# Performance work log

Measured on AMD Instinct MI355X. Metric: run time of the kernel, lower is better.

## Reference

```python
import jax, jax.numpy as jnp
import numpy as np

N_NODES = 50000
N_EDGES = 800000
F_IN = 128
HID = 128
N_CLASSES = 16
SELF_LOOP_W = 2.0  # improved=True -> self-loop fill value 2.0


def _glorot(key, fan_in, fan_out):
    scale = jnp.sqrt(6.0 / (fan_in + fan_out))
    return jax.random.uniform(key, (fan_in, fan_out), jnp.float32, -scale, scale)


def gcn_conv(x, W, b, src, dst, n):
    # PyG GCNConv (improved): out = D^{-1/2} (A + 2I) D^{-1/2} (x W) + b
    h = x @ W                                   # [N, F_out] dense transform
    deg = jnp.zeros((n,), x.dtype).at[dst].add(1.0) + SELF_LOOP_W  # in-degree + 2
    dinv = jax.lax.rsqrt(deg)                   # deg^{-1/2}
    norm = dinv[src] * dinv[dst]                # per-edge coefficient [E]
    msg = h[src] * norm[:, None]                # gather + scale [E, F_out]
    agg = jax.ops.segment_sum(msg, dst, num_segments=n)
    agg = agg + (SELF_LOOP_W * dinv * dinv)[:, None] * h  # self-loop term
    return agg + b


def setup_inputs() -> dict:
    key = jax.random.key(0)
    ks = jax.random.split(key, 10)
    x = jax.random.normal(ks[0], (N_NODES, F_IN), jnp.float32)
    edge_index = jax.random.randint(ks[1], (2, N_EDGES), 0, N_NODES, jnp.int64)
    return {
        "x": x,
        "edge_index": edge_index,
        "W0": _glorot(ks[2], F_IN, HID), "b0": jnp.zeros((HID,), jnp.float32),
        "W1": _glorot(ks[3], HID, HID),  "b1": jnp.zeros((HID,), jnp.float32),
        "W2": _glorot(ks[4], HID, HID),  "b2": jnp.zeros((HID,), jnp.float32),
        "W3": _glorot(ks[5], HID, N_CLASSES), "b3": jnp.zeros((N_CLASSES,), jnp.float32),
    }


def reference(x, edge_index, W0, b0, W1, b1, W2, b2, W3, b3):
    src, dst = edge_index[0], edge_index[1]
    # dropout is identity in eval mode
    h = jax.nn.relu(gcn_conv(x, W0, b0, src, dst, N_NODES))
    h = jax.nn.relu(gcn_conv(h, W1, b1, src, dst, N_NODES))
    h = jax.nn.relu(gcn_conv(h, W2, b2, src, dst, N_NODES))
    return jnp.tanh(gcn_conv(h, W3, b3, src, dst, N_NODES))
```

## Files before the change

### kernel.cpp

```cpp
#include <hip/hip_runtime.h>
#include <hip/hip_fp16.h>
#include <math.h>

#define N_NODES 50000
#define N_EDGES 800000
#define NB 782
#define CH 4096
#define CAP 2048
#define BUCKET_BLOCKS 196
#define CAST_BLOCKS 6250
#define PREPW_BLOCKS 192
#define FILL_GRID (NB + CAST_BLOCKS + PREPW_BLOCKS)
#define FB 1563

typedef _Float16 half8 __attribute__((ext_vector_type(8)));
typedef float floatx4 __attribute__((ext_vector_type(4)));
typedef unsigned uintx4 __attribute__((ext_vector_type(4)));

__global__ __launch_bounds__(256) void k_bucket(const int* __restrict__ src,
                                                const int* __restrict__ dst,
                                                int* __restrict__ gcur,
                                                unsigned* __restrict__ arena) {
    __shared__ int cntA[NB];
    __shared__ int lofs[NB];
    __shared__ int gbase[NB];
    __shared__ int part[256];
    __shared__ unsigned buf[CH];
    const int t = threadIdx.x;
    const int ebase = blockIdx.x * CH;
    const int chunkN = min(CH, N_EDGES - ebase);

    for (int i = t; i < NB; i += 256) cntA[i] = 0;
    __syncthreads();
    for (int i = t; i < chunkN; i += 256)
        atomicAdd(&cntA[dst[ebase + i] >> 6], 1);
    __syncthreads();
    int c[4];
    int s = 0;
#pragma unroll
    for (int q = 0; q < 4; ++q) {
        int idx = t * 4 + q;
        c[q] = (idx < NB) ? cntA[idx] : 0;
        s += c[q];
    }
    part[t] = s;
    __syncthreads();
    for (int d = 1; d < 256; d <<= 1) {
        int u = (t >= d) ? part[t - d] : 0;
        __syncthreads();
        part[t] += u;
        __syncthreads();
    }
    int run = (t > 0) ? part[t - 1] : 0;
#pragma unroll
    for (int q = 0; q < 4; ++q) {
        int idx = t * 4 + q;
        if (idx < NB) {
            lofs[idx] = run;
            run += c[q];
            gbase[idx] = (c[q] > 0) ? atomicAdd(&gcur[idx], c[q]) : 0;
            cntA[idx] = 0;
        }
    }
    __syncthreads();
    for (int i = t; i < chunkN; i += 256) {
        int d = dst[ebase + i];
        int sv = src[ebase + i];
        int b = d >> 6;
        int pos = atomicAdd(&cntA[b], 1);
        buf[lofs[b] + pos] = ((unsigned)d << 16) | (unsigned)sv;
    }
    __syncthreads();
    for (int i = t; i < chunkN; i += 256) {
        unsigned v = buf[i];
        int b = (int)(v >> 16) >> 6;
        int q = i - lofs[b];
        int p = gbase[b] + q;
        if (p < CAP) arena[((size_t)b << 11) + p] = v;
    }
}

__global__ __launch_bounds__(256) void k_fill3prep(
    const unsigned* __restrict__ arena, const int* __restrict__ gcur,
    unsigned* __restrict__ packed, float* __restrict__ dinv,
    unsigned short* __restrict__ eidx, const float* __restrict__ x,
    __half* __restrict__ xh, const float* __restrict__ W0,
    const float* __restrict__ W1, const float* __restrict__ W2,
    __half* __restrict__ WT) {
    const int t = threadIdx.x;
    if (blockIdx.x < NB) {
        const int b = blockIdx.x;
        __shared__ int cnt64[64];
        __shared__ int cur64[64];
        if (t < 64) cnt64[t] = 0;
        __syncthreads();
        const int seglen = min(gcur[b], CAP);
        const unsigned* seg = arena + ((size_t)b << 11);
        for (int i = t; i < seglen; i += 256)
            atomicAdd(&cnt64[(seg[i] >> 16) & 63], 1);
        __syncthreads();
        if (t < 64) {
            int v = cnt64[t];
            int p = v;
#pragma unroll
            for (int d = 1; d < 64; d <<= 1) {
                int u = __shfl_up(p, d, 64);
                if (t >= d) p += u;
            }
            int excl = p - v;
            int node = b * 64 + t;
            if (node < N_NODES) {
                packed[node] =
                    ((unsigned)((b << 11) + excl) << 11) | (unsigned)v;
                dinv[node] = rsqrtf((float)v + 2.0f);
            }
            cur64[t] = excl;
        }
        __syncthreads();
        const int base = b << 11;
        for (int i = t; i < seglen; i += 256) {
            unsigned v = seg[i];
            int d = (int)(v >> 16) & 63;
            int pos = atomicAdd(&cur64[d], 1);
            eidx[base + pos] = (unsigned short)(v & 0xFFFFu);
        }
    } else if (blockIdx.x < NB + CAST_BLOCKS) {
        int i = (blockIdx.x - NB) * 256 + t;
        float4 v = *(const float4*)&x[(size_t)i * 4];
        union { ushort4 u; __half h[4]; } p;
        p.h[0] = __float2half(v.x); p.h[1] = __float2half(v.y);
        p.h[2] = __float2half(v.z); p.h[3] = __float2half(v.w);
        *(ushort4*)&xh[(size_t)i * 4] = p.u;
    } else {
        int idx = blockIdx.x - NB - CAST_BLOCKS;
        int which = idx >> 6;
        const float* W = (which == 0) ? W0 : (which == 1) ? W1 : W2;
        int i = (idx & 63) * 256 + t;
        int k = i >> 7, n = i & 127;
        int np = ((n & 7) << 4) + (n >> 3);
        WT[which * 128 * 128 + np * 128 + k] = __float2half(W[i]);
    }
}

__device__ __forceinline__ void accs(uint4 ua, uint4 ub, float s, float* acc) {
    union { uint4 u; __half2 h2[4]; } va, vb;
    va.u = ua; vb.u = ub;
#pragma unroll
    for (int q = 0; q < 4; ++q) {
        float2 wa = __half22float2(va.h2[q]);
        float2 wb = __half22float2(vb.h2[q]);
        acc[2 * q]     += s * wa.x;
        acc[2 * q + 1] += s * wa.y;
        acc[8 + 2 * q]     += s * wb.x;
        acc[8 + 2 * q + 1] += s * wb.y;
    }
}

template <bool SC>
__global__ __launch_bounds__(256, 2) void k_fused(
    const __half* __restrict__ pin, const __half* __restrict__ WTl,
    const float* __restrict__ dinv, const unsigned* __restrict__ packed,
    const unsigned short* __restrict__ eidx, const float* __restrict__ bias,
    __half* __restrict__ pout) {
    __shared__ __half tl[32 * 136];
    const int t = threadIdx.x;
    const int node8 = t >> 3;
    const int l8 = t & 7;
    const int r = blockIdx.x * 32 + node8;
    const bool valid = r < N_NODES;

    float acc[16];
#pragma unroll
    for (int j = 0; j < 16; ++j) acc[j] = 0.f;
    int i = 0, end = 0;
    if (valid) {
        const uint4* rp = (const uint4*)&pin[(size_t)r * 128];
        uint4 sa = rp[l8], sb = rp[8 + l8];
        float s2 = SC ? 2.f * dinv[r] : 2.f;
        accs(sa, sb, s2, acc);
        unsigned pk = packed[r];
        i = (int)(pk >> 11);
        end = i + (int)(pk & 2047u);
    }
    for (; i + 8 <= end; i += 8) {
        int my = (int)__builtin_nontemporal_load(&eidx[i + l8]);
        uint4 va[8], vb[8];
        float ds8[8];
#pragma unroll
        for (int j = 0; j < 8; ++j) {
            int s0 = __shfl(my, j, 8);
            const uint4* q = (const uint4*)&pin[(size_t)s0 * 128];
            va[j] = q[l8];
            vb[j] = q[8 + l8];
            if (SC) ds8[j] = dinv[s0];
        }
#pragma unroll
        for (int j = 0; j < 8; ++j)
            accs(va[j], vb[j], SC ? ds8[j] : 1.f, acc);
    }
    if (i < end) {
        int n = end - i;
        int my = (l8 < n) ? (int)eidx[i + l8] : 0;
        for (int j = 0; j < n; ++j) {
            int s0 = __shfl(my, j, 8);
            const uint4* q = (const uint4*)&pin[(size_t)s0 * 128];
            accs(q[l8], q[8 + l8], SC ? dinv[s0] : 1.f, acc);
        }
    }
    {
        union { uintx4 u; __half h[8]; } pa, pb;
#pragma unroll
        for (int j = 0; j < 8; ++j) {
            pa.h[j] = __float2half(acc[j]);
            pb.h[j] = __float2half(acc[8 + j]);
        }
        *(uintx4*)&tl[node8 * 136 + 8 * l8] = pa.u;
        *(uintx4*)&tl[node8 * 136 + 64 + 8 * l8] = pb.u;
    }
    __syncthreads();

    const int wave = t >> 6;
    const int lane = t & 63;
    const int m = lane & 15;
    const int quad = lane >> 4;
    const int rtile = wave >> 1;
    const int ctile = wave & 1;
    floatx4 a4[4] = {};
#pragma unroll
    for (int kb = 0; kb < 4; ++kb) {
        half8 af = *(const half8*)&tl[(rtile * 16 + m) * 136 + quad * 8 + kb * 32];
#pragma unroll
        for (int j = 0; j < 4; ++j) {
            half8 bf = *(const half8*)&WTl[(size_t)(((ctile * 4 + j) * 16 + m)) * 128 +
                                           kb * 32 + quad * 8];
            a4[j] = __builtin_amdgcn_mfma_f32_16x16x32_f16(af, bf, a4[j], 0, 0, 0);
        }
    }
    const int f0 = 8 * m + ctile * 4;
    const float4 bi = *(const float4*)&bias[f0];
    const int nb0 = blockIdx.x * 32 + rtile * 16 + quad * 4;
#pragma unroll
    for (int rr = 0; rr < 4; ++rr) {
        int node = nb0 + rr;
        if (node < N_NODES) {
            float dv = dinv[node];
            union { ushort4 u; __half h[4]; } pk4;
            pk4.h[0] = __float2half(fmaxf(dv * (dv * a4[0][rr] + bi.x), 0.f));
            pk4.h[1] = __float2half(fmaxf(dv * (dv * a4[1][rr] + bi.y), 0.f));
            pk4.h[2] = __float2half(fmaxf(dv * (dv * a4[2][rr] + bi.z), 0.f));
            pk4.h[3] = __float2half(fmaxf(dv * (dv * a4[3][rr] + bi.w), 0.f));
            *(ushort4*)&pout[(size_t)node * 128 + f0] = pk4.u;
        }
    }
}

__global__ __launch_bounds__(256) void k_gemm16(const __half* __restrict__ in,
                                                const float* __restrict__ W,
                                                float* __restrict__ hs) {
    __shared__ float Wt[16 * 132];
    const int tid = threadIdx.x;
    for (int i = tid; i < 128 * 16; i += 256) {
        int k = i >> 4, c = i & 15;
        Wt[c * 132 + k] = W[i];
    }
    __syncthreads();
    int gid = blockIdx.x * 256 + tid;
    int r = gid >> 4, c = gid & 15;
    const __half* arow = &in[(size_t)r * 128];
    const float* wrow = &Wt[c * 132];
    float acc = 0.f;
#pragma unroll
    for (int k0 = 0; k0 < 128; k0 += 8) {
        union { uint4 u; __half2 h2[4]; } p;
        p.u = *(const uint4*)&arow[k0];
#pragma unroll
        for (int q = 0; q < 4; ++q) {
            float2 a = __half22float2(p.h2[q]);
            acc += a.x * wrow[k0 + 2 * q] + a.y * wrow[k0 + 2 * q + 1];
        }
    }
    hs[gid] = acc;
}

__global__ __launch_bounds__(256) void k_gather4(const unsigned* __restrict__ packed,
                                                 const unsigned short* __restrict__ eidx,
                                                 const float* __restrict__ hs,
                                                 const float* __restrict__ dinv,
                                                 const float* __restrict__ bias,
                                                 float* __restrict__ out) {
    int tid = blockIdx.x * 256 + threadIdx.x;
    int r = tid >> 2;
    if (r >= N_NODES) return;
    int l = tid & 3;
    int f = l * 4;
    const float dv = dinv[r];
    const float4 bi = *(const float4*)&bias[f];
    float4 h = *(const float4*)&hs[(size_t)r * 16 + f];
    float ax = 2.f * h.x, ay = 2.f * h.y, az = 2.f * h.z, aw = 2.f * h.w;
    unsigned pk = packed[r];
    int i = (int)(pk >> 11);
    int end = i + (int)(pk & 2047u);
    for (; i + 4 <= end; i += 4) {
        int my = (int)eidx[i + l];
#pragma unroll
        for (int j = 0; j < 4; ++j) {
            int s = __shfl(my, j, 4);
            float4 v = *(const float4*)&hs[(size_t)s * 16 + f];
            ax += v.x; ay += v.y; az += v.z; aw += v.w;
        }
    }
    if (i < end) {
        int n = end - i;
        int my = (l < n) ? (int)eidx[i + l] : 0;
        for (int j = 0; j < n; ++j) {
            int s = __shfl(my, j, 4);
            float4 v = *(const float4*)&hs[(size_t)s * 16 + f];
            ax += v.x; ay += v.y; az += v.z; aw += v.w;
        }
    }
    float v0 = tanhf(dv * ax + bi.x);
    float v1 = tanhf(dv * ay + bi.y);
    float v2 = tanhf(dv * az + bi.z);
    float v3 = tanhf(dv * aw + bi.w);
    floatx4 o = {v0, v1, v2, v3};
    __builtin_nontemporal_store(o, (floatx4*)&out[(size_t)r * 16 + f]);
}

extern "C" void kernel_launch(void* const* d_in, const int* in_sizes, int n_in,
                              void* d_out, int out_size, void* d_ws, size_t ws_size,
                              hipStream_t stream) {
    const float* x  = (const float*)d_in[0];
    const int* ei   = (const int*)d_in[1];
    const float* W0 = (const float*)d_in[2];
    const float* b0 = (const float*)d_in[3];
    const float* W1 = (const float*)d_in[4];
    const float* b1 = (const float*)d_in[5];
    const float* W2 = (const float*)d_in[6];
    const float* b2 = (const float*)d_in[7];
    const float* W3 = (const float*)d_in[8];
    const float* b3 = (const float*)d_in[9];
    const int* src = ei;
    const int* dst = ei + N_EDGES;

    __half* A      = (__half*)d_ws;
    __half* P      = A + (size_t)N_NODES * 128;
    __half* WT     = P + (size_t)N_NODES * 128;
    float*  H16    = (float*)(WT + 3 * 128 * 128);
    float*  dinv   = H16 + (size_t)N_NODES * 16;
    unsigned* packed = (unsigned*)(dinv + N_NODES);
    int*    gcur   = (int*)(packed + N_NODES);
    unsigned short* eidx = (unsigned short*)(gcur + 1024);
    unsigned* arena = (unsigned*)(eidx + NB * CAP);

    (void)hipMemsetAsync(gcur, 0, 1024 * sizeof(int), stream);
    k_bucket<<<BUCKET_BLOCKS, 256, 0, stream>>>(src, dst, gcur, arena);
    k_fill3prep<<<FILL_GRID, 256, 0, stream>>>(arena, gcur, packed, dinv,
                                               eidx, x, A, W0, W1, W2, WT);

    k_fused<true><<<FB, 256, 0, stream>>>(A, WT, dinv, packed, eidx, b0, P);
    k_fused<false><<<FB, 256, 0, stream>>>(P, WT + 128 * 128, dinv, packed,
                                           eidx, b1, A);
    k_fused<false><<<FB, 256, 0, stream>>>(A, WT + 2 * 128 * 128, dinv, packed,
                                           eidx, b2, P);
    k_gemm16<<<N_NODES * 16 / 256, 256, 0, stream>>>(P, W3, H16);
    k_gather4<<<(N_NODES * 4 + 255) / 256, 256, 0, stream>>>(
        packed, eidx, H16, dinv, b3, (float*)d_out);
}
```

Measured before the change: 287.8 us.

## Shrink fused aggregation blocks to 16 nodes with 16 lanes per node

The fused gather+GEMM kernel now handles 16 nodes per block instead of 32, giving each node 16 lanes that each load one 16-byte chunk. This halves the accumulator registers, and the launch-bounds occupancy hint rises from 2 to 8 blocks per SM, so more gather loads can be in flight at once. The MFMA stage is re-tiled so each wave computes two 16-column tiles. The grid doubles to 3125 blocks, which exactly covers 50000 nodes, so the bounds checks are removed. In exchange, each warp-wide gather touches fewer distinct rows, and per-block overhead (W loads, syncs) is amortized over fewer nodes.

```diff
diff --git a/kernel.cpp b/kernel.cpp
--- a/kernel.cpp
+++ b/kernel.cpp
@@ -11,7 +11,7 @@
 #define CAST_BLOCKS 6250
 #define PREPW_BLOCKS 192
 #define FILL_GRID (NB + CAST_BLOCKS + PREPW_BLOCKS)
-#define FB 1563
+#define FB 3125
 
 typedef _Float16 half8 __attribute__((ext_vector_type(8)));
 typedef float floatx4 __attribute__((ext_vector_type(4)));
@@ -142,80 +142,80 @@
     }
 }
 
-__device__ __forceinline__ void accs(uint4 ua, uint4 ub, float s, float* acc) {
-    union { uint4 u; __half2 h2[4]; } va, vb;
-    va.u = ua; vb.u = ub;
-#pragma unroll
-    for (int q = 0; q < 4; ++q) {
-        float2 wa = __half22float2(va.h2[q]);
-        float2 wb = __half22float2(vb.h2[q]);
-        acc[2 * q]     += s * wa.x;
-        acc[2 * q + 1] += s * wa.y;
-        acc[8 + 2 * q]     += s * wb.x;
-        acc[8 + 2 * q + 1] += s * wb.y;
-    }
-}
-
 template <bool SC>
-__global__ __launch_bounds__(256, 2) void k_fused(
+__global__ __launch_bounds__(256, 8) void k_fused(
     const __half* __restrict__ pin, const __half* __restrict__ WTl,
     const float* __restrict__ dinv, const unsigned* __restrict__ packed,
     const unsigned short* __restrict__ eidx, const float* __restrict__ bias,
     __half* __restrict__ pout) {
-    __shared__ __half tl[32 * 136];
+    __shared__ __half tl[16 * 136];
     const int t = threadIdx.x;
-    const int node8 = t >> 3;
-    const int l8 = t & 7;
-    const int r = blockIdx.x * 32 + node8;
-    const bool valid = r < N_NODES;
-
-    float acc[16];
-#pragma unroll
-    for (int j = 0; j < 16; ++j) acc[j] = 0.f;
-    int i = 0, end = 0;
-    if (valid) {
-        const uint4* rp = (const uint4*)&pin[(size_t)r * 128];
-        uint4 sa = rp[l8], sb = rp[8 + l8];
+    const int g = t >> 4;
+    const int l = t & 15;
+    const int r = blockIdx.x * 16 + g;
+    const int e8 = l & 7;
+
+    float acc[8];
+    {
+        uint4 sv = *(const uint4*)&pin[(size_t)r * 128 + l * 8];
         float s2 = SC ? 2.f * dinv[r] : 2.f;
-        accs(sa, sb, s2, acc);
-        unsigned pk = packed[r];
-        i = (int)(pk >> 11);
-        end = i + (int)(pk & 2047u);
-    }
+        union { uint4 u; __half2 h2[4]; } v;
+        v.u = sv;
+#pragma unroll
+        for (int q = 0; q < 4; ++q) {
+            float2 w = __half22float2(v.h2[q]);
+            acc[2 * q] = s2 * w.x;
+            acc[2 * q + 1] = s2 * w.y;
+        }
+    }
+    unsigned pk = packed[r];
+    int i = (int)(pk >> 11);
+    int end = i + (int)(pk & 2047u);
     for (; i + 8 <= end; i += 8) {
-        int my = (int)__builtin_nontemporal_load(&eidx[i + l8]);
-        uint4 va[8], vb[8];
+        int my = (int)__builtin_nontemporal_load(&eidx[i + e8]);
+        uint4 va[8];
         float ds8[8];
 #pragma unroll
         for (int j = 0; j < 8; ++j) {
-            int s0 = __shfl(my, j, 8);
-            const uint4* q = (const uint4*)&pin[(size_t)s0 * 128];
-            va[j] = q[l8];
-            vb[j] = q[8 + l8];
+            int s0 = __shfl(my, j, 16);
+            va[j] = *(const uint4*)&pin[(size_t)s0 * 128 + l * 8];
             if (SC) ds8[j] = dinv[s0];
         }
 #pragma unroll
-        for (int j = 0; j < 8; ++j)
-            accs(va[j], vb[j], SC ? ds8[j] : 1.f, acc);
+        for (int j = 0; j < 8; ++j) {
+            union { uint4 u; __half2 h2[4]; } v;
+            v.u = va[j];
+            float s = SC ? ds8[j] : 1.f;
+#pragma unroll
+            for (int q = 0; q < 4; ++q) {
+                float2 w = __half22float2(v.h2[q]);
+                acc[2 * q] += s * w.x;
+                acc[2 * q + 1] += s * w.y;
+            }
+        }
     }
     if (i < end) {
         int n = end - i;
-        int my = (l8 < n) ? (int)eidx[i + l8] : 0;
+        int my = (e8 < n) ? (int)eidx[i + e8] : 0;
         for (int j = 0; j < n; ++j) {
-            int s0 = __shfl(my, j, 8);
-            const uint4* q = (const uint4*)&pin[(size_t)s0 * 128];
-            accs(q[l8], q[8 + l8], SC ? dinv[s0] : 1.f, acc);
+            int s0 = __shfl(my, j, 16);
+            uint4 u = *(const uint4*)&pin[(size_t)s0 * 128 + l * 8];
+            float s = SC ? dinv[s0] : 1.f;
+            union { uint4 uu; __half2 h2[4]; } v;
+            v.uu = u;
+#pragma unroll
+            for (int q = 0; q < 4; ++q) {
+                float2 w = __half22float2(v.h2[q]);
+                acc[2 * q] += s * w.x;
+                acc[2 * q + 1] += s * w.y;
+            }
         }
     }
     {
-        union { uintx4 u; __half h[8]; } pa, pb;
-#pragma unroll
-        for (int j = 0; j < 8; ++j) {
-            pa.h[j] = __float2half(acc[j]);
-            pb.h[j] = __float2half(acc[8 + j]);
-        }
-        *(uintx4*)&tl[node8 * 136 + 8 * l8] = pa.u;
-        *(uintx4*)&tl[node8 * 136 + 64 + 8 * l8] = pb.u;
+        union { uintx4 u; __half h[8]; } p;
+#pragma unroll
+        for (int j = 0; j < 8; ++j) p.h[j] = __float2half(acc[j]);
+        *(uintx4*)&tl[g * 136 + l * 8] = p.u;
     }
     __syncthreads();
 
@@ -223,34 +223,28 @@
     const int lane = t & 63;
     const int m = lane & 15;
     const int quad = lane >> 4;
-    const int rtile = wave >> 1;
-    const int ctile = wave & 1;
-    floatx4 a4[4] = {};
+    floatx4 a4[2] = {};
 #pragma unroll
     for (int kb = 0; kb < 4; ++kb) {
-        half8 af = *(const half8*)&tl[(rtile * 16 + m) * 136 + quad * 8 + kb * 32];
-#pragma unroll
-        for (int j = 0; j < 4; ++j) {
-            half8 bf = *(const half8*)&WTl[(size_t)(((ctile * 4 + j) * 16 + m)) * 128 +
+        half8 af = *(const half8*)&tl[m * 136 + quad * 8 + kb * 32];
+#pragma unroll
+        for (int j = 0; j < 2; ++j) {
+            half8 bf = *(const half8*)&WTl[(size_t)((2 * wave + j) * 16 + m) * 128 +
                                            kb * 32 + quad * 8];
             a4[j] = __builtin_amdgcn_mfma_f32_16x16x32_f16(af, bf, a4[j], 0, 0, 0);
         }
     }
-    const int f0 = 8 * m + ctile * 4;
-    const float4 bi = *(const float4*)&bias[f0];
-    const int nb0 = blockIdx.x * 32 + rtile * 16 + quad * 4;
+    const int f0 = 8 * m + 2 * wave;
+    const float2 bi = *(const float2*)&bias[f0];
+    const int nb0 = blockIdx.x * 16 + quad * 4;
 #pragma unroll
     for (int rr = 0; rr < 4; ++rr) {
         int node = nb0 + rr;
-        if (node < N_NODES) {
-            float dv = dinv[node];
-            union { ushort4 u; __half h[4]; } pk4;
-            pk4.h[0] = __float2half(fmaxf(dv * (dv * a4[0][rr] + bi.x), 0.f));
-            pk4.h[1] = __float2half(fmaxf(dv * (dv * a4[1][rr] + bi.y), 0.f));
-            pk4.h[2] = __float2half(fmaxf(dv * (dv * a4[2][rr] + bi.z), 0.f));
-            pk4.h[3] = __float2half(fmaxf(dv * (dv * a4[3][rr] + bi.w), 0.f));
-            *(ushort4*)&pout[(size_t)node * 128 + f0] = pk4.u;
-        }
+        float dv = dinv[node];
+        union { unsigned u; __half h[2]; } o;
+        o.h[0] = __float2half(fmaxf(dv * (dv * a4[0][rr] + bi.x), 0.f));
+        o.h[1] = __float2half(fmaxf(dv * (dv * a4[1][rr] + bi.y), 0.f));
+        *(unsigned*)&pout[(size_t)node * 128 + f0] = o.u;
     }
 }
 
```

After: 335.9 us. 1.17x slower.

## Fuse final 128x16 GEMM into layer-3 kernel and move casts into bucket kernel

Applied to the files above, without the earlier changes.

The third GCN layer kernel now also runs the last 128->16 projection with MFMA on its activated tile held in shared memory. It writes H16 directly, so the layer-3 fp16 output no longer makes a global round trip and the separate k_gemm16 launch is gone. The x cast and weight transposes (now including an fp16 transposed W3) move from the fill kernel into the bucket kernel's grid, so they run alongside bucketing. The shared gather loop also drops the nontemporal load hint on edge indices, and the last-layer projection now uses fp16 inputs instead of fp32 weights.

```diff
diff --git a/kernel.cpp b/kernel.cpp
--- a/kernel.cpp
+++ b/kernel.cpp
@@ -10,23 +10,53 @@
 #define BUCKET_BLOCKS 196
 #define CAST_BLOCKS 6250
 #define PREPW_BLOCKS 192
-#define FILL_GRID (NB + CAST_BLOCKS + PREPW_BLOCKS)
+#define W3_BLOCKS 8
+#define BPREP_GRID (BUCKET_BLOCKS + CAST_BLOCKS + PREPW_BLOCKS + W3_BLOCKS)
 #define FB 1563
 
 typedef _Float16 half8 __attribute__((ext_vector_type(8)));
 typedef float floatx4 __attribute__((ext_vector_type(4)));
 typedef unsigned uintx4 __attribute__((ext_vector_type(4)));
 
-__global__ __launch_bounds__(256) void k_bucket(const int* __restrict__ src,
-                                                const int* __restrict__ dst,
-                                                int* __restrict__ gcur,
-                                                unsigned* __restrict__ arena) {
+__global__ __launch_bounds__(256) void k_bucket_prep(
+    const int* __restrict__ src, const int* __restrict__ dst,
+    int* __restrict__ gcur, unsigned* __restrict__ arena,
+    const float* __restrict__ x, __half* __restrict__ xh,
+    const float* __restrict__ W0, const float* __restrict__ W1,
+    const float* __restrict__ W2, const float* __restrict__ W3,
+    __half* __restrict__ WT, __half* __restrict__ WT3) {
+    const int t = threadIdx.x;
+    if (blockIdx.x >= BUCKET_BLOCKS) {
+        int xb = blockIdx.x - BUCKET_BLOCKS;
+        if (xb < CAST_BLOCKS) {
+            int i = xb * 256 + t;
+            float4 v = *(const float4*)&x[(size_t)i * 4];
+            union { ushort4 u; __half h[4]; } p;
+            p.h[0] = __float2half(v.x); p.h[1] = __float2half(v.y);
+            p.h[2] = __float2half(v.z); p.h[3] = __float2half(v.w);
+            *(ushort4*)&xh[(size_t)i * 4] = p.u;
+        } else {
+            int idx = xb - CAST_BLOCKS;
+            if (idx < PREPW_BLOCKS) {
+                int which = idx >> 6;
+                const float* W = (which == 0) ? W0 : (which == 1) ? W1 : W2;
+                int i = (idx & 63) * 256 + t;
+                int k = i >> 7, n = i & 127;
+                int np = ((n & 7) << 4) + (n >> 3);
+                WT[which * 128 * 128 + np * 128 + k] = __float2half(W[i]);
+            } else {
+                int i = (idx - PREPW_BLOCKS) * 256 + t;
+                int n = i >> 7, k = i & 127;
+                WT3[n * 128 + k] = __float2half(W3[k * 16 + n]);
+            }
+        }
+        return;
+    }
     __shared__ int cntA[NB];
     __shared__ int lofs[NB];
     __shared__ int gbase[NB];
     __shared__ int part[256];
     __shared__ unsigned buf[CH];
-    const int t = threadIdx.x;
     const int ebase = blockIdx.x * CH;
     const int chunkN = min(CH, N_EDGES - ebase);
 
@@ -80,65 +110,44 @@
     }
 }
 
-__global__ __launch_bounds__(256) void k_fill3prep(
+__global__ __launch_bounds__(256) void k_fill(
     const unsigned* __restrict__ arena, const int* __restrict__ gcur,
     unsigned* __restrict__ packed, float* __restrict__ dinv,
-    unsigned short* __restrict__ eidx, const float* __restrict__ x,
-    __half* __restrict__ xh, const float* __restrict__ W0,
-    const float* __restrict__ W1, const float* __restrict__ W2,
-    __half* __restrict__ WT) {
+    unsigned short* __restrict__ eidx) {
     const int t = threadIdx.x;
-    if (blockIdx.x < NB) {
-        const int b = blockIdx.x;
-        __shared__ int cnt64[64];
-        __shared__ int cur64[64];
-        if (t < 64) cnt64[t] = 0;
-        __syncthreads();
-        const int seglen = min(gcur[b], CAP);
-        const unsigned* seg = arena + ((size_t)b << 11);
-        for (int i = t; i < seglen; i += 256)
-            atomicAdd(&cnt64[(seg[i] >> 16) & 63], 1);
-        __syncthreads();
-        if (t < 64) {
-            int v = cnt64[t];
-            int p = v;
-#pragma unroll
-            for (int d = 1; d < 64; d <<= 1) {
-                int u = __shfl_up(p, d, 64);
-                if (t >= d) p += u;
-            }
-            int excl = p - v;
-            int node = b * 64 + t;
-            if (node < N_NODES) {
-                packed[node] =
-                    ((unsigned)((b << 11) + excl) << 11) | (unsigned)v;
-                dinv[node] = rsqrtf((float)v + 2.0f);
-            }
-            cur64[t] = excl;
-        }
-        __syncthreads();
-        const int base = b << 11;
-        for (int i = t; i < seglen; i += 256) {
-            unsigned v = seg[i];
-            int d = (int)(v >> 16) & 63;
-            int pos = atomicAdd(&cur64[d], 1);
-            eidx[base + pos] = (unsigned short)(v & 0xFFFFu);
-        }
-    } else if (blockIdx.x < NB + CAST_BLOCKS) {
-        int i = (blockIdx.x - NB) * 256 + t;
-        float4 v = *(const float4*)&x[(size_t)i * 4];
-        union { ushort4 u; __half h[4]; } p;
-        p.h[0] = __float2half(v.x); p.h[1] = __float2half(v.y);
-        p.h[2] = __float2half(v.z); p.h[3] = __float2half(v.w);
-        *(ushort4*)&xh[(size_t)i * 4] = p.u;
-    } else {
-        int idx = blockIdx.x - NB - CAST_BLOCKS;
-        int which = idx >> 6;
-        const float* W = (which == 0) ? W0 : (which == 1) ? W1 : W2;
-        int i = (idx & 63) * 256 + t;
-        int k = i >> 7, n = i & 127;
-        int np = ((n & 7) << 4) + (n >> 3);
-        WT[which * 128 * 128 + np * 128 + k] = __float2half(W[i]);
+    const int b = blockIdx.x;
+    __shared__ int cnt64[64];
+    __shared__ int cur64[64];
+    if (t < 64) cnt64[t] = 0;
+    __syncthreads();
+    const int seglen = min(gcur[b], CAP);
+    const unsigned* seg = arena + ((size_t)b << 11);
+    for (int i = t; i < seglen; i += 256)
+        atomicAdd(&cnt64[(seg[i] >> 16) & 63], 1);
+    __syncthreads();
+    if (t < 64) {
+        int v = cnt64[t];
+        int p = v;
+#pragma unroll
+        for (int d = 1; d < 64; d <<= 1) {
+            int u = __shfl_up(p, d, 64);
+            if (t >= d) p += u;
+        }
+        int excl = p - v;
+        int node = b * 64 + t;
+        if (node < N_NODES) {
+            packed[node] = ((unsigned)((b << 11) + excl) << 11) | (unsigned)v;
+            dinv[node] = rsqrtf((float)v + 2.0f);
+        }
+        cur64[t] = excl;
+    }
+    __syncthreads();
+    const int base = b << 11;
+    for (int i = t; i < seglen; i += 256) {
+        unsigned v = seg[i];
+        int d = (int)(v >> 16) & 63;
+        int pos = atomicAdd(&cur64[d], 1);
+        eidx[base + pos] = (unsigned short)(v & 0xFFFFu);
     }
 }
 
@@ -153,6 +162,50 @@
         acc[2 * q + 1] += s * wa.y;
         acc[8 + 2 * q]     += s * wb.x;
         acc[8 + 2 * q + 1] += s * wb.y;
+    }
+}
+
+template <bool SC>
+__device__ __forceinline__ void gather_stage(
+    int r, bool valid, int l8, const __half* __restrict__ pin,
+    const float* __restrict__ dinv, const unsigned* __restrict__ packed,
+    const unsigned short* __restrict__ eidx, float* acc) {
+#pragma unroll
+    for (int j = 0; j < 16; ++j) acc[j] = 0.f;
+    int i = 0, end = 0;
+    if (valid) {
+        const uint4* rp = (const uint4*)&pin[(size_t)r * 128];
+        uint4 sa = rp[l8], sb = rp[8 + l8];
+        float s2 = SC ? 2.f * dinv[r] : 2.f;
+        accs(sa, sb, s2, acc);
+        unsigned pk = packed[r];
+        i = (int)(pk >> 11);
+        end = i + (int)(pk & 2047u);
+    }
+    for (; i + 8 <= end; i += 8) {
+        int my = (int)eidx[i + l8];
+        uint4 va[8], vb[8];
+        float ds8[8];
+#pragma unroll
+        for (int j = 0; j < 8; ++j) {
+            int s0 = __shfl(my, j, 8);
+            const uint4* q = (const uint4*)&pin[(size_t)s0 * 128];
+            va[j] = q[l8];
+            vb[j] = q[8 + l8];
+            if (SC) ds8[j] = dinv[s0];
+        }
+#pragma unroll
+        for (int j = 0; j < 8; ++j)
+            accs(va[j], vb[j], SC ? ds8[j] : 1.f, acc);
+    }
+    if (i < end) {
+        int n = end - i;
+        int my = (l8 < n) ? (int)eidx[i + l8] : 0;
+        for (int j = 0; j < n; ++j) {
+            int s0 = __shfl(my, j, 8);
+            const uint4* q = (const uint4*)&pin[(size_t)s0 * 128];
+            accs(q[l8], q[8 + l8], SC ? dinv[s0] : 1.f, acc);
+        }
     }
 }
 
@@ -167,46 +220,10 @@
     const int node8 = t >> 3;
     const int l8 = t & 7;
     const int r = blockIdx.x * 32 + node8;
-    const bool valid = r < N_NODES;
 
     float acc[16];
-#pragma unroll
-    for (int j = 0; j < 16; ++j) acc[j] = 0.f;
-    int i = 0, end = 0;
-    if (valid) {
-        const uint4* rp = (const uint4*)&pin[(size_t)r * 128];
-        uint4 sa = rp[l8], sb = rp[8 + l8];
-        float s2 = SC ? 2.f * dinv[r] : 2.f;
-        accs(sa, sb, s2, acc);
-        unsigned pk = packed[r];
-        i = (int)(pk >> 11);
-        end = i + (int)(pk & 2047u);
-    }
-    for (; i + 8 <= end; i += 8) {
-        int my = (int)__builtin_nontemporal_load(&eidx[i + l8]);
-        uint4 va[8], vb[8];
-        float ds8[8];
-#pragma unroll
-        for (int j = 0; j < 8; ++j) {
-            int s0 = __shfl(my, j, 8);
-            const uint4* q = (const uint4*)&pin[(size_t)s0 * 128];
-            va[j] = q[l8];
-            vb[j] = q[8 + l8];
-            if (SC) ds8[j] = dinv[s0];
-        }
-#pragma unroll
-        for (int j = 0; j < 8; ++j)
-            accs(va[j], vb[j], SC ? ds8[j] : 1.f, acc);
-    }
-    if (i < end) {
-        int n = end - i;
-        int my = (l8 < n) ? (int)eidx[i + l8] : 0;
-        for (int j = 0; j < n; ++j) {
-            int s0 = __shfl(my, j, 8);
-            const uint4* q = (const uint4*)&pin[(size_t)s0 * 128];
-            accs(q[l8], q[8 + l8], SC ? dinv[s0] : 1.f, acc);
-        }
-    }
+    gather_stage<SC>(r, r < N_NODES, l8, pin, dinv, packed, eidx, acc);
+
     {
         union { uintx4 u; __half h[8]; } pa, pb;
 #pragma unroll
@@ -254,32 +271,81 @@
     }
 }
 
-__global__ __launch_bounds__(256) void k_gemm16(const __half* __restrict__ in,
-                                                const float* __restrict__ W,
-                                                float* __restrict__ hs) {
-    __shared__ float Wt[16 * 132];
-    const int tid = threadIdx.x;
-    for (int i = tid; i < 128 * 16; i += 256) {
-        int k = i >> 4, c = i & 15;
-        Wt[c * 132 + k] = W[i];
-    }
-    __syncthreads();
-    int gid = blockIdx.x * 256 + tid;
-    int r = gid >> 4, c = gid & 15;
-    const __half* arow = &in[(size_t)r * 128];
-    const float* wrow = &Wt[c * 132];
-    float acc = 0.f;
-#pragma unroll
-    for (int k0 = 0; k0 < 128; k0 += 8) {
-        union { uint4 u; __half2 h2[4]; } p;
-        p.u = *(const uint4*)&arow[k0];
-#pragma unroll
-        for (int q = 0; q < 4; ++q) {
-            float2 a = __half22float2(p.h2[q]);
-            acc += a.x * wrow[k0 + 2 * q] + a.y * wrow[k0 + 2 * q + 1];
-        }
-    }
-    hs[gid] = acc;
+__global__ __launch_bounds__(256, 2) void k_fused_last(
+    const __half* __restrict__ pin, const __half* __restrict__ WTl,
+    const __half* __restrict__ WT3, const float* __restrict__ dinv,
+    const unsigned* __restrict__ packed, const unsigned short* __restrict__ eidx,
+    const float* __restrict__ bias, float* __restrict__ H16) {
+    __shared__ __half tl[32 * 136];
+    const int t = threadIdx.x;
+    const int node8 = t >> 3;
+    const int l8 = t & 7;
+    const int r = blockIdx.x * 32 + node8;
+
+    float acc[16];
+    gather_stage<false>(r, r < N_NODES, l8, pin, dinv, packed, eidx, acc);
+
+    {
+        union { uintx4 u; __half h[8]; } pa, pb;
+#pragma unroll
+        for (int j = 0; j < 8; ++j) {
+            pa.h[j] = __float2half(acc[j]);
+            pb.h[j] = __float2half(acc[8 + j]);
+        }
+        *(uintx4*)&tl[node8 * 136 + 8 * l8] = pa.u;
+        *(uintx4*)&tl[node8 * 136 + 64 + 8 * l8] = pb.u;
+    }
+    __syncthreads();
+
+    const int wave = t >> 6;
+    const int lane = t & 63;
+    const int m = lane & 15;
+    const int quad = lane >> 4;
+    const int rtile = wave >> 1;
+    const int ctile = wave & 1;
+    floatx4 a4[4] = {};
+#pragma unroll
+    for (int kb = 0; kb < 4; ++kb) {
+        half8 af = *(const half8*)&tl[(rtile * 16 + m) * 136 + quad * 8 + kb * 32];
+#pragma unroll
+        for (int j = 0; j < 4; ++j) {
+            half8 bf = *(const half8*)&WTl[(size_t)(((ctile * 4 + j) * 16 + m)) * 128 +
+                                           kb * 32 + quad * 8];
+            a4[j] = __builtin_amdgcn_mfma_f32_16x16x32_f16(af, bf, a4[j], 0, 0, 0);
+        }
+    }
+    __syncthreads();
+
+    const int f0 = 8 * m + ctile * 4;
+    const float4 bi = *(const float4*)&bias[f0];
+    const int rowb = rtile * 16 + quad * 4;
+#pragma unroll
+    for (int rr = 0; rr < 4; ++rr) {
+        int node = blockIdx.x * 32 + rowb + rr;
+        float dv = (node < N_NODES) ? dinv[node] : 0.f;
+        union { ushort4 u; __half h[4]; } pk4;
+        pk4.h[0] = __float2half(fmaxf(dv * (dv * a4[0][rr] + bi.x), 0.f));
+        pk4.h[1] = __float2half(fmaxf(dv * (dv * a4[1][rr] + bi.y), 0.f));
+        pk4.h[2] = __float2half(fmaxf(dv * (dv * a4[2][rr] + bi.z), 0.f));
+        pk4.h[3] = __float2half(fmaxf(dv * (dv * a4[3][rr] + bi.w), 0.f));
+        *(ushort4*)&tl[(rowb + rr) * 136 + f0] = pk4.u;
+    }
+    __syncthreads();
+
+    if (wave < 2) {
+        floatx4 c2 = {};
+#pragma unroll
+        for (int kb = 0; kb < 4; ++kb) {
+            half8 af2 = *(const half8*)&tl[(wave * 16 + m) * 136 + quad * 8 + kb * 32];
+            half8 bf2 = *(const half8*)&WT3[(size_t)m * 128 + kb * 32 + quad * 8];
+            c2 = __builtin_amdgcn_mfma_f32_16x16x32_f16(af2, bf2, c2, 0, 0, 0);
+        }
+#pragma unroll
+        for (int rr = 0; rr < 4; ++rr) {
+            int node = blockIdx.x * 32 + wave * 16 + quad * 4 + rr;
+            if (node < N_NODES) H16[(size_t)node * 16 + m] = c2[rr];
+        }
+    }
 }
 
 __global__ __launch_bounds__(256) void k_gather4(const unsigned* __restrict__ packed,
@@ -345,7 +411,8 @@
     __half* A      = (__half*)d_ws;
     __half* P      = A + (size_t)N_NODES * 128;
     __half* WT     = P + (size_t)N_NODES * 128;
-    float*  H16    = (float*)(WT + 3 * 128 * 128);
+    __half* WT3    = WT + 3 * 128 * 128;
+    float*  H16    = (float*)(WT3 + 16 * 128);
     float*  dinv   = H16 + (size_t)N_NODES * 16;
     unsigned* packed = (unsigned*)(dinv + N_NODES);
     int*    gcur   = (int*)(packed + N_NODES);
@@ -353,16 +420,15 @@
     unsigned* arena = (unsigned*)(eidx + NB * CAP);
 
     (void)hipMemsetAsync(gcur, 0, 1024 * sizeof(int), stream);
-    k_bucket<<<BUCKET_BLOCKS, 256, 0, stream>>>(src, dst, gcur, arena);
-    k_fill3prep<<<FILL_GRID, 256, 0, stream>>>(arena, gcur, packed, dinv,
-                                               eidx, x, A, W0, W1, W2, WT);
+    k_bucket_prep<<<BPREP_GRID, 256, 0, stream>>>(src, dst, gcur, arena, x, A,
+                                                  W0, W1, W2, W3, WT, WT3);
+    k_fill<<<NB, 256, 0, stream>>>(arena, gcur, packed, dinv, eidx);
 
     k_fused<true><<<FB, 256, 0, stream>>>(A, WT, dinv, packed, eidx, b0, P);
     k_fused<false><<<FB, 256, 0, stream>>>(P, WT + 128 * 128, dinv, packed,
                                            eidx, b1, A);
-    k_fused<false><<<FB, 256, 0, stream>>>(A, WT + 2 * 128 * 128, dinv, packed,
-                                           eidx, b2, P);
-    k_gemm16<<<N_NODES * 16 / 256, 256, 0, stream>>>(P, W3, H16);
+    k_fused_last<<<FB, 256, 0, stream>>>(A, WT + 2 * 128 * 128, WT3, dinv,
+                                         packed, eidx, b2, H16);
     k_gather4<<<(N_NODES * 4 + 255) / 256, 256, 0, stream>>>(
         packed, eidx, H16, dinv, b3, (float*)d_out);
 }
```

New measurement: 255.0 us. -11.4%, faster.
